# Optimization experiments

Measured on AMD Instinct MI355X. Metric: run time of the kernel, lower is better.

The kernel has to match this reference:

```python
import jax, jax.numpy as jnp
import numpy as np

N1, N2, C, G1, G2 = 20000, 80000, 64, 128, 256
K = 27


def _nbr_map(coords, key, G):
    # coords sorted by key = x*G*G + y*G + z; returns [M,27] neighbor idx, -1 if absent
    M = coords.shape[0]
    nbr = np.full((M, K), -1, np.int32)
    k = 0
    for dx in (-1, 0, 1):
        for dy in (-1, 0, 1):
            for dz in (-1, 0, 1):
                nc = coords + np.array([dx, dy, dz])
                valid = np.all((nc >= 0) & (nc < G), axis=1)
                nk = nc[:, 0] * G * G + nc[:, 1] * G + nc[:, 2]
                pos = np.clip(np.searchsorted(key, nk), 0, M - 1)
                hit = valid & (key[pos] == nk)
                nbr[:, k] = np.where(hit, pos, -1)
                k += 1
    return nbr


def setup_inputs() -> dict:
    rng = np.random.default_rng(0)
    # --- parent (curr) level: unique sorted voxels on 128^3 grid ---
    lin = np.sort(rng.choice(G1 ** 3, size=N1, replace=False))
    cc = np.stack([lin // (G1 * G1), (lin // G1) % G1, lin % G1], axis=1)
    # occupancy codes with exactly 4 set bits -> exactly 4 children per parent
    bits4 = np.argsort(rng.random((N1, 8)), axis=1)[:, :4]  # [N1,4]
    curr_occ = (1 << bits4).sum(axis=1).astype(np.int32)[:, None]
    # --- FCG expansion: child coords = parent*2 + octant offset ---
    off = np.stack([(bits4 >> 2) & 1, (bits4 >> 1) & 1, bits4 & 1], axis=-1)
    child = (cc[:, None, :] * 2 + off).reshape(-1, 3)
    parent_idx = np.repeat(np.arange(N1, dtype=np.int32), 4)
    ckey = child[:, 0] * G2 * G2 + child[:, 1] * G2 + child[:, 2]
    o = np.argsort(ckey)  # op.sort_CF
    child, parent_idx, ckey = child[o], parent_idx[o], ckey[o]
    next_octant = ((child[:, 0] % 2) * 4 + (child[:, 1] % 2) * 2 + (child[:, 2] % 2)).astype(np.int32)
    next_occ = rng.integers(0, 256, size=(N2, 1)).astype(np.int32)
    nbr_curr = _nbr_map(cc, lin, G1)
    nbr_next = _nbr_map(child, ckey, G2)

    key = jax.random.key(0)
    ks = jax.random.split(key, 16)
    f32 = jnp.float32
    inp = {
        'prior_emb': jax.random.normal(ks[0], (256, C), f32),
        'target_emb8': jax.random.normal(ks[1], (8, C), f32),
        'Wp': jax.random.normal(ks[2], (5, K, C, C), f32) * 0.03,
        'Wt': jax.random.normal(ks[3], (5, K, C, C), f32) * 0.03,
        'W0a': jax.random.normal(ks[4], (C, C), f32) * 0.1,
        'b0a': jnp.zeros((C,), f32),
        'W0b': jax.random.normal(ks[5], (C, 16), f32) * 0.1,
        'b0b': jnp.zeros((16,), f32),
        'W1a': jax.random.normal(ks[6], (C, C), f32) * 0.1,
        'b1a': jnp.zeros((C,), f32),
        'W1b': jax.random.normal(ks[7], (C, 16), f32) * 0.1,
        'b1b': jnp.zeros((16,), f32),
        's1_emb': jax.random.normal(ks[8], (16, C), f32),
        'curr_occ': jnp.asarray(curr_occ),
        'next_occ': jnp.asarray(next_occ),
        'next_octant': jnp.asarray(next_octant),
        'parent_idx': jnp.asarray(parent_idx),
        'nbr_curr': jnp.asarray(nbr_curr),
        'nbr_next': jnp.asarray(nbr_next),
        'n_points': 640000,
    }
    return inp


def _sp_conv(feats, nbr, W):
    # 3x3x3 sparse conv via kernel map: out[i] = sum_k feats[nbr[i,k]] @ W[k]
    out = jnp.zeros((feats.shape[0], W.shape[-1]), feats.dtype)
    for k in range(K):
        idx = nbr[:, k]
        g = jnp.where((idx >= 0)[:, None], feats[jnp.clip(idx, 0, None)], 0.0)
        out = out + g @ W[k]
    return out


def _resnet(feats, nbr, Wa, Wb):
    h = jax.nn.relu(_sp_conv(feats, nbr, Wa))
    h = _sp_conv(h, nbr, Wb)
    return jax.nn.relu(feats + h)


def reference(prior_emb, target_emb8, Wp, Wt, W0a, b0a, W0b, b0b, W1a, b1a, W1b, b1b, s1_emb,
              curr_occ, next_occ, next_octant, parent_idx, nbr_curr, nbr_next, n_points):
    # prior branch on parent level
    f = prior_emb[curr_occ[:, 0]]                              # [N1,C]
    f = jax.nn.relu(_sp_conv(f, nbr_curr, Wp[0]))
    f = _resnet(f, nbr_curr, Wp[1], Wp[2])
    f = _resnet(f, nbr_curr, Wp[3], Wp[4])
    # FCG: broadcast parent feats to children, add octant (target) embedding
    g = f[parent_idx] + target_emb8[next_octant]               # [N2,C]
    g = jax.nn.relu(_sp_conv(g, nbr_next, Wt[0]))
    g = _resnet(g, nbr_next, Wt[1], Wt[2])
    g = _resnet(g, nbr_next, Wt[3], Wt[4])
    # bit-prediction heads
    lower = jnp.remainder(next_occ, 16)                        # [N2,1]
    upper = next_occ // 16                                     # [N2,1]
    lp = jax.nn.softmax(jax.nn.relu(g @ W0a + b0a) @ W0b + b0b, axis=-1)
    h1 = g + s1_emb[lower[:, 0]]
    up = jax.nn.softmax(jax.nn.relu(h1 @ W1a + b1a) @ W1b + b1b, axis=-1)
    lp_gt = jnp.take_along_axis(lp, lower, axis=1)
    up_gt = jnp.take_along_axis(up, upper, axis=1)
    eps = 1e-10
    bits = jnp.sum(jnp.clip(-jnp.log2(lp_gt + eps), 0.0, 50.0))
    bits = bits + jnp.sum(jnp.clip(-jnp.log2(up_gt + eps), 0.0, 50.0))
    return bits / n_points
```

## Files before the change

### kernel.cpp

```cpp
#include <hip/hip_runtime.h>

#define NP1 20000
#define NP2 80000
#define KN  27

typedef unsigned short ushort;
typedef unsigned int   uint;
typedef __attribute__((ext_vector_type(8))) short short8v;
typedef __attribute__((ext_vector_type(4))) float f32x4;

__device__ __forceinline__ ushort f2bf(float x) {
    union { float f; uint u; } v; v.f = x;
    uint r = v.u + 0x7fffu + ((v.u >> 16) & 1u);
    return (ushort)(r >> 16);
}
__device__ __forceinline__ float bf2f(ushort s) {
    union { uint u; float f; } v; v.u = ((uint)s) << 16;
    return v.f;
}
__device__ __forceinline__ void gload_lds16(const void* g, void* l) {
    __builtin_amdgcn_global_load_lds(
        (const __attribute__((address_space(1))) unsigned int*)g,
        (__attribute__((address_space(3))) unsigned int*)l, 16, 0, 0);
}
__device__ __forceinline__ int xcd_swz(int b, int nb) {
    int q = nb >> 3, r = nb & 7;
    int x = b & 7, p = b >> 3;
    return (x < r) ? x * (q + 1) + p : r * (q + 1) + (x - r) * q + p;
}

__global__ __launch_bounds__(256) void prep_wT_tile_k(
    const float* __restrict__ Wp, const float* __restrict__ Wt,
    ushort* __restrict__ dstp, ushort* __restrict__ dstt)
{
    __shared__ float sT[64 * 65];
    int b = blockIdx.x;
    const float* W = (b < 135) ? Wp : Wt;
    ushort* dst    = (b < 135) ? dstp : dstt;
    int k = (b < 135) ? b : b - 135;
    const float* src = W + (size_t)k * 4096;
    int t = threadIdx.x;
    #pragma unroll
    for (int p = 0; p < 16; ++p) {
        int i = t + p * 256;
        sT[(i >> 6) * 65 + (i & 63)] = src[i];
    }
    __syncthreads();
    ushort* d = dst + (size_t)k * 4096;
    #pragma unroll
    for (int p = 0; p < 16; ++p) {
        int o = t + p * 256;
        int c = o >> 6, jj = o & 63;
        int j = (((jj >> 3) ^ (c & 7)) << 3) | (jj & 7);
        d[o] = f2bf(sT[j * 65 + c]);
    }
}

__global__ __launch_bounds__(256) void prep_small_k(
    const float* __restrict__ W0a, const float* __restrict__ W1a,
    const float* __restrict__ W0b, const float* __restrict__ W1b,
    const float* __restrict__ s1,
    ushort* __restrict__ W0aT, ushort* __restrict__ W1aT,
    ushort* __restrict__ W0bT, ushort* __restrict__ W1bT,
    ushort* __restrict__ s1bT)
{
    int b = blockIdx.x, t = threadIdx.x;
    if (b < 32) {
        const float* W = (b < 16) ? W0a : W1a;
        ushort* dst    = (b < 16) ? W0aT : W1aT;
        int i = (b & 15) * 256 + t;
        int c = i >> 6, jj = i & 63;
        int j = (((jj >> 3) ^ (c & 7)) << 3) | (jj & 7);
        dst[i] = f2bf(W[j * 64 + c]);
    } else if (b < 40) {
        const float* W = (b < 36) ? W0b : W1b;
        ushort* dst    = (b < 36) ? W0bT : W1bT;
        int i = (b - ((b < 36) ? 32 : 36)) * 256 + t;
        int c = i >> 6, jj = i & 63;
        int j = (((jj >> 3) ^ (c & 7)) << 3) | (jj & 7);
        dst[i] = f2bf(W[j * 16 + c]);
    } else {
        int i = (b - 40) * 256 + t;
        int e = i >> 6, jj = i & 63;
        int j = (((jj >> 3) ^ (e & 7)) << 3) | (jj & 7);
        s1bT[i] = f2bf(s1[e * 64 + j]);
    }
}

__global__ __launch_bounds__(256) void gather_curr_k(
    const float* __restrict__ prior_emb, const int* __restrict__ curr_occ,
    ushort* __restrict__ out)
{
    int i = blockIdx.x * 256 + threadIdx.x;
    if (i >= NP1 * 32) return;
    int row = i >> 5, cp = (i & 31) * 2;
    const float* src = prior_emb + (size_t)curr_occ[row] * 64 + cp;
    uint pk = (uint)f2bf(src[0]) | ((uint)f2bf(src[1]) << 16);
    *(uint*)((char*)out + (size_t)row * 128 + cp * 2) = pk;
}

__global__ __launch_bounds__(256) void gather_next_k(
    const ushort* __restrict__ f, const int* __restrict__ parent_idx,
    const int* __restrict__ next_oct, const float* __restrict__ temb8,
    ushort* __restrict__ out)
{
    int i = blockIdx.x * 256 + threadIdx.x;
    if (i >= NP2 * 32) return;
    int row = i >> 5, cp = (i & 31) * 2;
    const ushort* fs = f + (size_t)parent_idx[row] * 64 + cp;
    const float* ts = temb8 + (size_t)next_oct[row] * 64 + cp;
    float v0 = bf2f(fs[0]) + ts[0];
    float v1 = bf2f(fs[1]) + ts[1];
    uint pk = (uint)f2bf(v0) | ((uint)f2bf(v1) << 16);
    *(uint*)((char*)out + (size_t)row * 128 + cp * 2) = pk;
}

template<int NW, int CG>
__global__ __launch_bounds__(NW * 64) void spconv_reg_k(
    const ushort* __restrict__ feats, const int* __restrict__ nbr,
    const ushort* __restrict__ Wsw, const ushort* __restrict__ res,
    ushort* __restrict__ out, const ushort* __restrict__ zpage, int nblocks)
{
    constexpr int ROWS   = (NW / CG) * 16;
    constexpr int NB     = 4 / CG;
    constexpr int WLOADS = 8192 / (NW * 64 * 16);

    __shared__ __align__(16) char sW[2 * 8192];

    const int t = threadIdx.x;
    const int w = t >> 6, l = t & 63;
    const int wg = xcd_swz(blockIdx.x, nblocks);
    const int row0 = wg * ROWS;
    const int lr = l & 15, lhi = l >> 4;
    const int colbase = (w % CG) * (NB * 16);
    const int rw = w / CG;
    const int ch0 = lhi ^ (lr & 7);
    const int ch1 = (4 + lhi) ^ (lr & 7);

    const int* nbrow = nbr + (size_t)(row0 + rw * 16 + lr) * KN;

    f32x4 acc[NB];
    #pragma unroll
    for (int b = 0; b < NB; ++b) acc[b] = (f32x4)0.0f;

    short8v aC0, aC1, aN0, aN1;
    int idxA, idxB;

    #define LOADA(IDX, CHOFF) \
        (*(const short8v*)(((IDX) >= 0 ? (const char*)feats + (size_t)(IDX) * 128 \
                                       : (const char*)zpage) + ((CHOFF) + lhi) * 16))

    {
        int id0 = nbrow[0];
        aC0 = LOADA(id0, 0);
        aC1 = LOADA(id0, 4);
        idxA = nbrow[1];
        const char* wsrc = (const char*)Wsw;
        #pragma unroll
        for (int i = 0; i < WLOADS; ++i) {
            int off = (w * WLOADS + i) * 1024;
            gload_lds16(wsrc + off + l * 16, sW + off);
        }
    }

    for (int k = 0; k < KN; ++k) {
        char* cur = sW + (k & 1) * 8192;
        char* nxt = sW + ((k + 1) & 1) * 8192;

        __syncthreads();

        if (k < KN - 1) {
            const char* wsrc = (const char*)Wsw + (size_t)(k + 1) * 8192;
            #pragma unroll
            for (int i = 0; i < WLOADS; ++i) {
                int off = (w * WLOADS + i) * 1024;
                gload_lds16(wsrc + off + l * 16, nxt + off);
            }
            aN0 = LOADA(idxA, 0);
            aN1 = LOADA(idxA, 4);
        }
        if (k < KN - 2) idxB = nbrow[k + 2];

        __builtin_amdgcn_s_setprio(1);
        {
            short8v b0[NB];
            #pragma unroll
            for (int nb = 0; nb < NB; ++nb)
                b0[nb] = *(const short8v*)(cur + (colbase + nb * 16 + lr) * 128 + ch0 * 16);
            #pragma unroll
            for (int nb = 0; nb < NB; ++nb)
                acc[nb] = __builtin_amdgcn_mfma_f32_16x16x32_bf16(aC0, b0[nb], acc[nb], 0, 0, 0);
            short8v b1[NB];
            #pragma unroll
            for (int nb = 0; nb < NB; ++nb)
                b1[nb] = *(const short8v*)(cur + (colbase + nb * 16 + lr) * 128 + ch1 * 16);
            #pragma unroll
            for (int nb = 0; nb < NB; ++nb)
                acc[nb] = __builtin_amdgcn_mfma_f32_16x16x32_bf16(aC1, b1[nb], acc[nb], 0, 0, 0);
        }
        __builtin_amdgcn_s_setprio(0);

        aC0 = aN0; aC1 = aN1; idxA = idxB;
    }
    #undef LOADA

    #pragma unroll
    for (int nb = 0; nb < NB; ++nb) {
        #pragma unroll
        for (int r = 0; r < 4; ++r) {
            int rg = row0 + rw * 16 + lhi * 4 + r;
            int c = colbase + nb * 16 + lr;
            float v = acc[nb][r];
            if (res != nullptr) v += bf2f(res[(size_t)rg * 64 + c]);
            v = fmaxf(v, 0.0f);
            float o = __shfl_xor(v, 1);
            if (!(l & 1)) {
                uint pk = (uint)f2bf(v) | ((uint)f2bf(o) << 16);
                *(uint*)((char*)out + (size_t)rg * 128 + (c << 1)) = pk;
            }
        }
    }
}

__global__ __launch_bounds__(512) void head_v2_k(
    const ushort* __restrict__ G, const int* __restrict__ next_occ,
    const ushort* __restrict__ Wsmall,
    const float* __restrict__ b0a, const float* __restrict__ b1a,
    const float* __restrict__ b0b, const float* __restrict__ b1b,
    const int* __restrict__ n_points, float* __restrict__ outp)
{
    __shared__ __align__(16) char sm[48288];
    char*  sWs = sm;
    char*  sHb = sm + 22528;
    float* sLb = (float*)(sm + 38912);
    float* sBf = (float*)(sm + 47616);
    float* sRed = (float*)(sm + 48256);

    const int t = threadIdx.x;
    const int w = t >> 6, l = t & 63;
    const int row0 = blockIdx.x * 128;
    const int lr = l & 15, lhi = l >> 4;
    char*  sH = sHb + w * 2048;
    float* sL = sLb + w * 272;

    const int myrow = row0 + w * 16 + lr;
    const int occ_l = next_occ[myrow];

    short8v aG0 = *(const short8v*)((const char*)G + (size_t)myrow * 128 + lhi * 16);
    short8v aG1 = *(const short8v*)((const char*)G + (size_t)myrow * 128 + (4 + lhi) * 16);

    for (int i = w; i < 22; i += 8)
        gload_lds16((const char*)Wsmall + i * 1024 + l * 16, sWs + i * 1024);
    if (t < 64)       sBf[t] = b0a[t];
    else if (t < 128) sBf[t] = b1a[t - 64];
    else if (t < 144) sBf[128 + (t - 128)] = b0b[t - 128];
    else if (t < 160) sBf[144 + (t - 144)] = b1b[t - 144];
    __syncthreads();

    float bacc = 0.0f;

    {
        f32x4 a0[4];
        #pragma unroll
        for (int b = 0; b < 4; ++b) a0[b] = (f32x4)0.0f;
        #pragma unroll
        for (int j0 = 0; j0 < 2; ++j0) {
            short8v a = j0 ? aG1 : aG0;
            #pragma unroll
            for (int nb = 0; nb < 4; ++nb) {
                int c = nb * 16 + lr;
                int ch = (j0 * 4 + lhi) ^ (c & 7);
                short8v b = *(const short8v*)(sWs + c * 128 + ch * 16);
                a0[nb] = __builtin_amdgcn_mfma_f32_16x16x32_bf16(a, b, a0[nb], 0, 0, 0);
            }
        }
        #pragma unroll
        for (int nb = 0; nb < 4; ++nb) {
            float bias = sBf[nb * 16 + lr];
            #pragma unroll
            for (int r = 0; r < 4; ++r) {
                int row = lhi * 4 + r;
                int j = nb * 16 + lr;
                float v = fmaxf(a0[nb][r] + bias, 0.0f);
                float o = __shfl_xor(v, 1);
                if (!(l & 1)) {
                    uint pk = (uint)f2bf(v) | ((uint)f2bf(o) << 16);
                    *(uint*)(sH + row * 128 + (((j >> 3) ^ (row & 7)) << 4)
                             + (j & 7) * 2) = pk;
                }
            }
        }
        asm volatile("s_waitcnt lgkmcnt(0)" ::: "memory");
        __builtin_amdgcn_sched_barrier(0);
        f32x4 lg = (f32x4)0.0f;
        #pragma unroll
        for (int j0 = 0; j0 < 2; ++j0) {
            int ch = (j0 * 4 + lhi) ^ (lr & 7);
            short8v a = *(const short8v*)(sH + lr * 128 + ch * 16);
            short8v b = *(const short8v*)(sWs + 16384 + lr * 128 + ch * 16);
            lg = __builtin_amdgcn_mfma_f32_16x16x32_bf16(a, b, lg, 0, 0, 0);
        }
        #pragma unroll
        for (int r = 0; r < 4; ++r)
            sL[(lhi * 4 + r) * 17 + lr] = lg[r] + sBf[128 + lr];
        asm volatile("s_waitcnt lgkmcnt(0)" ::: "memory");
        __builtin_amdgcn_sched_barrier(0);
        {
            int tgt = occ_l & 15;
            float lv[16], mx = -1e30f;
            #pragma unroll
            for (int c = 0; c < 16; ++c) {
                lv[c] = sL[lr * 17 + c];
                mx = fmaxf(mx, lv[c]);
            }
            float ssum = 0.0f, lt = lv[0];
            #pragma unroll
            for (int c = 0; c < 16; ++c) {
                ssum += __expf(lv[c] - mx);
                lt = (c == tgt) ? lv[c] : lt;
            }
            float p = __expf(lt - mx) / ssum;
            float bits = fminf(fmaxf(-log2f(p + 1e-10f), 0.0f), 50.0f);
            if (l < 16) bacc += bits;
        }
    }

    {
        f32x4 a1[4];
        #pragma unroll
        for (int b = 0; b < 4; ++b) a1[b] = (f32x4)0.0f;
        int low_l = occ_l & 15;
        #pragma unroll
        for (int j0 = 0; j0 < 2; ++j0) {
            short8v g8 = j0 ? aG1 : aG0;
            int che = (j0 * 4 + lhi) ^ (low_l & 7);
            short8v e8 = *(const short8v*)(sWs + 20480 + low_l * 128 + che * 16);
            short8v a;
            #pragma unroll
            for (int e = 0; e < 8; ++e) {
                float f = bf2f((ushort)g8[e]) + bf2f((ushort)e8[e]);
                a[e] = (short)f2bf(f);
            }
            #pragma unroll
            for (int nb = 0; nb < 4; ++nb) {
                int c = nb * 16 + lr;
                int ch = (j0 * 4 + lhi) ^ (c & 7);
                short8v b = *(const short8v*)(sWs + 8192 + c * 128 + ch * 16);
                a1[nb] = __builtin_amdgcn_mfma_f32_16x16x32_bf16(a, b, a1[nb], 0, 0, 0);
            }
        }
        #pragma unroll
        for (int nb = 0; nb < 4; ++nb) {
            float bias = sBf[64 + nb * 16 + lr];
            #pragma unroll
            for (int r = 0; r < 4; ++r) {
                int row = lhi * 4 + r;
                int j = nb * 16 + lr;
                float v = fmaxf(a1[nb][r] + bias, 0.0f);
                float o = __shfl_xor(v, 1);
                if (!(l & 1)) {
                    uint pk = (uint)f2bf(v) | ((uint)f2bf(o) << 16);
                    *(uint*)(sH + row * 128 + (((j >> 3) ^ (row & 7)) << 4)
                             + (j & 7) * 2) = pk;
                }
            }
        }
        asm volatile("s_waitcnt lgkmcnt(0)" ::: "memory");
        __builtin_amdgcn_sched_barrier(0);
        f32x4 lg = (f32x4)0.0f;
        #pragma unroll
        for (int j0 = 0; j0 < 2; ++j0) {
            int ch = (j0 * 4 + lhi) ^ (lr & 7);
            short8v a = *(const short8v*)(sH + lr * 128 + ch * 16);
            short8v b = *(const short8v*)(sWs + 18432 + lr * 128 + ch * 16);
            lg = __builtin_amdgcn_mfma_f32_16x16x32_bf16(a, b, lg, 0, 0, 0);
        }
        #pragma unroll
        for (int r = 0; r < 4; ++r)
            sL[(lhi * 4 + r) * 17 + lr] = lg[r] + sBf[144 + lr];
        asm volatile("s_waitcnt lgkmcnt(0)" ::: "memory");
        __builtin_amdgcn_sched_barrier(0);
        {
            int tgt = occ_l >> 4;
            float lv[16], mx = -1e30f;
            #pragma unroll
            for (int c = 0; c < 16; ++c) {
                lv[c] = sL[lr * 17 + c];
                mx = fmaxf(mx, lv[c]);
            }
            float ssum = 0.0f, lt = lv[0];
            #pragma unroll
            for (int c = 0; c < 16; ++c) {
                ssum += __expf(lv[c] - mx);
                lt = (c == tgt) ? lv[c] : lt;
            }
            float p = __expf(lt - mx) / ssum;
            float bits = fminf(fmaxf(-log2f(p + 1e-10f), 0.0f), 50.0f);
            if (l < 16) bacc += bits;
        }
    }

    #pragma unroll
    for (int s = 1; s < 64; s <<= 1) bacc += __shfl_xor(bacc, s);
    if (l == 0) sRed[w] = bacc;
    __syncthreads();
    if (t == 0) {
        float s = 0.0f;
        #pragma unroll
        for (int i = 0; i < 8; ++i) s += sRed[i];
        atomicAdd(outp, s / (float)(*n_points));
    }
}

extern "C" void kernel_launch(void* const* d_in, const int* in_sizes, int n_in,
                              void* d_out, int out_size, void* d_ws, size_t ws_size,
                              hipStream_t stream)
{
    const float* prior_emb = (const float*)d_in[0];
    const float* temb8     = (const float*)d_in[1];
    const float* Wp        = (const float*)d_in[2];
    const float* Wt        = (const float*)d_in[3];
    const float* W0a       = (const float*)d_in[4];
    const float* b0a       = (const float*)d_in[5];
    const float* W0b       = (const float*)d_in[6];
    const float* b0b       = (const float*)d_in[7];
    const float* W1a       = (const float*)d_in[8];
    const float* b1a       = (const float*)d_in[9];
    const float* W1b       = (const float*)d_in[10];
    const float* b1b       = (const float*)d_in[11];
    const float* s1_emb    = (const float*)d_in[12];
    const int*   curr_occ  = (const int*)d_in[13];
    const int*   next_occ  = (const int*)d_in[14];
    const int*   next_oct  = (const int*)d_in[15];
    const int*   parent    = (const int*)d_in[16];
    const int*   nbr_curr  = (const int*)d_in[17];
    const int*   nbr_next  = (const int*)d_in[18];
    const int*   n_points  = (const int*)d_in[19];
    float* out = (float*)d_out;

    char* wsb = (char*)d_ws;
    ushort* zpage = (ushort*)wsb;
    size_t off = 256;
    ushort* WpT = (ushort*)(wsb + off); off += (size_t)135 * 4096 * 2;
    ushort* WtT = (ushort*)(wsb + off); off += (size_t)135 * 4096 * 2;
    ushort* Wsmall = (ushort*)(wsb + off);
    ushort* W0aT = Wsmall;
    ushort* W1aT = Wsmall + 4096;
    ushort* W0bT = Wsmall + 8192;
    ushort* W1bT = Wsmall + 9216;
    ushort* s1bT = Wsmall + 10240;
    off += 11264 * 2;
    off = (off + 255) & ~(size_t)255;
    ushort* fA = (ushort*)(wsb + off); off += (size_t)NP1 * 64 * 2;
    ushort* fB = (ushort*)(wsb + off); off += (size_t)NP1 * 64 * 2;
    ushort* fC = (ushort*)(wsb + off); off += (size_t)NP1 * 64 * 2;
    ushort* gA = (ushort*)(wsb + off); off += (size_t)NP2 * 64 * 2;
    ushort* gB = (ushort*)(wsb + off); off += (size_t)NP2 * 64 * 2;
    ushort* gC = (ushort*)(wsb + off); off += (size_t)NP2 * 64 * 2;

    hipMemsetAsync(d_out, 0, sizeof(float), stream);
    hipMemsetAsync(zpage, 0, 256, stream);

    prep_wT_tile_k<<<270, 256, 0, stream>>>(Wp, Wt, WpT, WtT);
    prep_small_k<<<44, 256, 0, stream>>>(W0a, W1a, W0b, W1b, s1_emb,
                                         W0aT, W1aT, W0bT, W1bT, s1bT);

    gather_curr_k<<<(NP1 * 32 + 255) / 256, 256, 0, stream>>>(prior_emb, curr_occ, fA);

    const size_t WT = (size_t)KN * 4096;
    spconv_reg_k<4,2><<<625, 256, 0, stream>>>(fA, nbr_curr, WpT + 0 * WT, nullptr, fB, zpage, 625);
    spconv_reg_k<4,2><<<625, 256, 0, stream>>>(fB, nbr_curr, WpT + 1 * WT, nullptr, fC, zpage, 625);
    spconv_reg_k<4,2><<<625, 256, 0, stream>>>(fC, nbr_curr, WpT + 2 * WT, fB,      fA, zpage, 625);
    spconv_reg_k<4,2><<<625, 256, 0, stream>>>(fA, nbr_curr, WpT + 3 * WT, nullptr, fC, zpage, 625);
    spconv_reg_k<4,2><<<625, 256, 0, stream>>>(fC, nbr_curr, WpT + 4 * WT, fA,      fB, zpage, 625);

    gather_next_k<<<(NP2 * 32 + 255) / 256, 256, 0, stream>>>(fB, parent, next_oct, temb8, gA);

    spconv_reg_k<8,1><<<625, 512, 0, stream>>>(gA, nbr_next, WtT + 0 * WT, nullptr, gB, zpage, 625);
    spconv_reg_k<8,1><<<625, 512, 0, stream>>>(gB, nbr_next, WtT + 1 * WT, nullptr, gC, zpage, 625);
    spconv_reg_k<8,1><<<625, 512, 0, stream>>>(gC, nbr_next, WtT + 2 * WT, gB,      gA, zpage, 625);
    spconv_reg_k<8,1><<<625, 512, 0, stream>>>(gA, nbr_next, WtT + 3 * WT, nullptr, gC, zpage, 625);
    spconv_reg_k<8,1><<<625, 512, 0, stream>>>(gC, nbr_next, WtT + 4 * WT, gA,      gB, zpage, 625);

    head_v2_k<<<625, 512, 0, stream>>>(gB, next_occ, Wsmall,
                                       b0a, b1a, b0b, b1b, n_points, out);
}
```

Baseline: 258.8 us.

## Load sparse-conv weights directly from global into registers, dropping LDS staging

The sparse convolution kernel stops staging per-offset weight tiles in LDS with double buffering and block-wide barriers. Each wave now loads its B fragments straight from global memory (which should stay L2-resident) into registers, using a two-stage even/odd software pipeline across the 27 kernel offsets. The next-level convs switch to 256-thread blocks with twice as many blocks, and the kernel gets an occupancy hint of 4 blocks per CU. This removes the barriers and LDS traffic but raises global/L2 load traffic and register pressure, since every wave fetches the weights itself.

Measured after the change: 646.0 us. 150% more time.

```diff
diff --git a/kernel.cpp b/kernel.cpp
--- a/kernel.cpp
+++ b/kernel.cpp
@@ -115,17 +115,14 @@
     *(uint*)((char*)out + (size_t)row * 128 + cp * 2) = pk;
 }
 
-template<int NW, int CG>
-__global__ __launch_bounds__(NW * 64) void spconv_reg_k(
+template<int CG>
+__global__ __launch_bounds__(256, 4) void spconv_nolds_k(
     const ushort* __restrict__ feats, const int* __restrict__ nbr,
     const ushort* __restrict__ Wsw, const ushort* __restrict__ res,
     ushort* __restrict__ out, const ushort* __restrict__ zpage, int nblocks)
 {
-    constexpr int ROWS   = (NW / CG) * 16;
-    constexpr int NB     = 4 / CG;
-    constexpr int WLOADS = 8192 / (NW * 64 * 16);
-
-    __shared__ __align__(16) char sW[2 * 8192];
+    constexpr int NB   = 4 / CG;
+    constexpr int ROWS = (4 / CG) * 16;
 
     const int t = threadIdx.x;
     const int w = t >> 6, l = t & 63;
@@ -134,75 +131,77 @@
     const int lr = l & 15, lhi = l >> 4;
     const int colbase = (w % CG) * (NB * 16);
     const int rw = w / CG;
-    const int ch0 = lhi ^ (lr & 7);
-    const int ch1 = (4 + lhi) ^ (lr & 7);
-
-    const int* nbrow = nbr + (size_t)(row0 + rw * 16 + lr) * KN;
+    const int myrow = row0 + rw * 16 + lr;
+    const int* nbrow = nbr + (size_t)myrow * KN;
+    const char* wbase = (const char*)Wsw;
+
+    int boff[2][NB];
+    #pragma unroll
+    for (int j0 = 0; j0 < 2; ++j0)
+        #pragma unroll
+        for (int nb = 0; nb < NB; ++nb) {
+            int c = colbase + nb * 16 + lr;
+            boff[j0][nb] = c * 128 + (((j0 * 4 + lhi) ^ (c & 7)) << 4);
+        }
 
     f32x4 acc[NB];
     #pragma unroll
     for (int b = 0; b < NB; ++b) acc[b] = (f32x4)0.0f;
 
-    short8v aC0, aC1, aN0, aN1;
-    int idxA, idxB;
+    short8v Ae0, Ae1, Ao0, Ao1;
+    short8v Be[2][NB], Bo[2][NB];
+    int idxO, idxE;
 
     #define LOADA(IDX, CHOFF) \
         (*(const short8v*)(((IDX) >= 0 ? (const char*)feats + (size_t)(IDX) * 128 \
                                        : (const char*)zpage) + ((CHOFF) + lhi) * 16))
+    #define LOADB(DST, K)                                                        \
+        _Pragma("unroll")                                                        \
+        for (int j0 = 0; j0 < 2; ++j0)                                           \
+            _Pragma("unroll")                                                    \
+            for (int nb = 0; nb < NB; ++nb)                                      \
+                DST[j0][nb] = *(const short8v*)(wbase + (size_t)(K) * 8192       \
+                                                + boff[j0][nb]);
+    #define COMPUTE(A0, A1, B)                                                   \
+        __builtin_amdgcn_s_setprio(1);                                           \
+        _Pragma("unroll")                                                        \
+        for (int nb = 0; nb < NB; ++nb)                                          \
+            acc[nb] = __builtin_amdgcn_mfma_f32_16x16x32_bf16(A0, B[0][nb],      \
+                                                              acc[nb], 0, 0, 0); \
+        _Pragma("unroll")                                                        \
+        for (int nb = 0; nb < NB; ++nb)                                          \
+            acc[nb] = __builtin_amdgcn_mfma_f32_16x16x32_bf16(A1, B[1][nb],      \
+                                                              acc[nb], 0, 0, 0); \
+        __builtin_amdgcn_s_setprio(0);
 
     {
         int id0 = nbrow[0];
-        aC0 = LOADA(id0, 0);
-        aC1 = LOADA(id0, 4);
-        idxA = nbrow[1];
-        const char* wsrc = (const char*)Wsw;
-        #pragma unroll
-        for (int i = 0; i < WLOADS; ++i) {
-            int off = (w * WLOADS + i) * 1024;
-            gload_lds16(wsrc + off + l * 16, sW + off);
-        }
-    }
-
-    for (int k = 0; k < KN; ++k) {
-        char* cur = sW + (k & 1) * 8192;
-        char* nxt = sW + ((k + 1) & 1) * 8192;
-
-        __syncthreads();
-
-        if (k < KN - 1) {
-            const char* wsrc = (const char*)Wsw + (size_t)(k + 1) * 8192;
-            #pragma unroll
-            for (int i = 0; i < WLOADS; ++i) {
-                int off = (w * WLOADS + i) * 1024;
-                gload_lds16(wsrc + off + l * 16, nxt + off);
-            }
-            aN0 = LOADA(idxA, 0);
-            aN1 = LOADA(idxA, 4);
-        }
-        if (k < KN - 2) idxB = nbrow[k + 2];
-
-        __builtin_amdgcn_s_setprio(1);
-        {
-            short8v b0[NB];
-            #pragma unroll
-            for (int nb = 0; nb < NB; ++nb)
-                b0[nb] = *(const short8v*)(cur + (colbase + nb * 16 + lr) * 128 + ch0 * 16);
-            #pragma unroll
-            for (int nb = 0; nb < NB; ++nb)
-                acc[nb] = __builtin_amdgcn_mfma_f32_16x16x32_bf16(aC0, b0[nb], acc[nb], 0, 0, 0);
-            short8v b1[NB];
-            #pragma unroll
-            for (int nb = 0; nb < NB; ++nb)
-                b1[nb] = *(const short8v*)(cur + (colbase + nb * 16 + lr) * 128 + ch1 * 16);
-            #pragma unroll
-            for (int nb = 0; nb < NB; ++nb)
-                acc[nb] = __builtin_amdgcn_mfma_f32_16x16x32_bf16(aC1, b1[nb], acc[nb], 0, 0, 0);
-        }
-        __builtin_amdgcn_s_setprio(0);
-
-        aC0 = aN0; aC1 = aN1; idxA = idxB;
-    }
+        Ae0 = LOADA(id0, 0);
+        Ae1 = LOADA(id0, 4);
+        LOADB(Be, 0);
+        idxO = nbrow[1];
+        idxE = nbrow[2];
+    }
+
+    #pragma unroll 1
+    for (int kp = 0; kp < 13; ++kp) {
+        const int k = 2 * kp;
+        Ao0 = LOADA(idxO, 0);
+        Ao1 = LOADA(idxO, 4);
+        LOADB(Bo, k + 1);
+        if (kp < 12) idxO = nbrow[k + 3];
+        COMPUTE(Ae0, Ae1, Be);
+        Ae0 = LOADA(idxE, 0);
+        Ae1 = LOADA(idxE, 4);
+        LOADB(Be, k + 2);
+        if (kp < 12) idxE = nbrow[k + 4];
+        COMPUTE(Ao0, Ao1, Bo);
+    }
+    COMPUTE(Ae0, Ae1, Be);
+
     #undef LOADA
+    #undef LOADB
+    #undef COMPUTE
 
     #pragma unroll
     for (int nb = 0; nb < NB; ++nb) {
@@ -468,19 +467,19 @@
     gather_curr_k<<<(NP1 * 32 + 255) / 256, 256, 0, stream>>>(prior_emb, curr_occ, fA);
 
     const size_t WT = (size_t)KN * 4096;
-    spconv_reg_k<4,2><<<625, 256, 0, stream>>>(fA, nbr_curr, WpT + 0 * WT, nullptr, fB, zpage, 625);
-    spconv_reg_k<4,2><<<625, 256, 0, stream>>>(fB, nbr_curr, WpT + 1 * WT, nullptr, fC, zpage, 625);
-    spconv_reg_k<4,2><<<625, 256, 0, stream>>>(fC, nbr_curr, WpT + 2 * WT, fB,      fA, zpage, 625);
-    spconv_reg_k<4,2><<<625, 256, 0, stream>>>(fA, nbr_curr, WpT + 3 * WT, nullptr, fC, zpage, 625);
-    spconv_reg_k<4,2><<<625, 256, 0, stream>>>(fC, nbr_curr, WpT + 4 * WT, fA,      fB, zpage, 625);
+    spconv_nolds_k<2><<<625, 256, 0, stream>>>(fA, nbr_curr, WpT + 0 * WT, nullptr, fB, zpage, 625);
+    spconv_nolds_k<2><<<625, 256, 0, stream>>>(fB, nbr_curr, WpT + 1 * WT, nullptr, fC, zpage, 625);
+    spconv_nolds_k<2><<<625, 256, 0, stream>>>(fC, nbr_curr, WpT + 2 * WT, fB,      fA, zpage, 625);
+    spconv_nolds_k<2><<<625, 256, 0, stream>>>(fA, nbr_curr, WpT + 3 * WT, nullptr, fC, zpage, 625);
+    spconv_nolds_k<2><<<625, 256, 0, stream>>>(fC, nbr_curr, WpT + 4 * WT, fA,      fB, zpage, 625);
 
     gather_next_k<<<(NP2 * 32 + 255) / 256, 256, 0, stream>>>(fB, parent, next_oct, temb8, gA);
 
-    spconv_reg_k<8,1><<<625, 512, 0, stream>>>(gA, nbr_next, WtT + 0 * WT, nullptr, gB, zpage, 625);
-    spconv_reg_k<8,1><<<625, 512, 0, stream>>>(gB, nbr_next, WtT + 1 * WT, nullptr, gC, zpage, 625);
-    spconv_reg_k<8,1><<<625, 512, 0, stream>>>(gC, nbr_next, WtT + 2 * WT, gB,      gA, zpage, 625);
-    spconv_reg_k<8,1><<<625, 512, 0, stream>>>(gA, nbr_next, WtT + 3 * WT, nullptr, gC, zpage, 625);
-    spconv_reg_k<8,1><<<625, 512, 0, stream>>>(gC, nbr_next, WtT + 4 * WT, gA,      gB, zpage, 625);
+    spconv_nolds_k<1><<<1250, 256, 0, stream>>>(gA, nbr_next, WtT + 0 * WT, nullptr, gB, zpage, 1250);
+    spconv_nolds_k<1><<<1250, 256, 0, stream>>>(gB, nbr_next, WtT + 1 * WT, nullptr, gC, zpage, 1250);
+    spconv_nolds_k<1><<<1250, 256, 0, stream>>>(gC, nbr_next, WtT + 2 * WT, gB,      gA, zpage, 1250);
+    spconv_nolds_k<1><<<1250, 256, 0, stream>>>(gA, nbr_next, WtT + 3 * WT, nullptr, gC, zpage, 1250);
+    spconv_nolds_k<1><<<1250, 256, 0, stream>>>(gC, nbr_next, WtT + 4 * WT, gA,      gB, zpage, 1250);
 
     head_v2_k<<<625, 512, 0, stream>>>(gB, next_occ, Wsmall,
                                        b0a, b1a, b0b, b1b, n_points, out);
```

## Add triple-buffered weight pipeline kernel for next-level sparse convs

Applied to the files above, without the earlier changes.

Adds a new sparse-conv kernel for the 80k-row level. It triple-buffers the per-tap weight tiles in LDS and prefetches neighbour feature rows two taps ahead, using explicit vmcnt waits and one barrier per tap. The aim is to hide global load latency for both weights and gathered features behind the MFMA work, replacing the previous double-buffered scheme. It costs more LDS and registers per block, which may lower occupancy. The existing kernel also gains an MB template parameter, which is set to 1 everywhere.

Result: slower. 296.7 us (+14.6%).

```diff
diff --git a/kernel.cpp b/kernel.cpp
--- a/kernel.cpp
+++ b/kernel.cpp
@@ -22,6 +22,12 @@
     __builtin_amdgcn_global_load_lds(
         (const __attribute__((address_space(1))) unsigned int*)g,
         (__attribute__((address_space(3))) unsigned int*)l, 16, 0, 0);
+}
+template<int N> __device__ __forceinline__ void wait_vmcnt() {
+    if constexpr (N == 0)      asm volatile("s_waitcnt vmcnt(0)" ::: "memory");
+    else if constexpr (N == 2) asm volatile("s_waitcnt vmcnt(2)" ::: "memory");
+    else if constexpr (N == 4) asm volatile("s_waitcnt vmcnt(4)" ::: "memory");
+    else if constexpr (N == 5) asm volatile("s_waitcnt vmcnt(5)" ::: "memory");
 }
 __device__ __forceinline__ int xcd_swz(int b, int nb) {
     int q = nb >> 3, r = nb & 7;
@@ -115,13 +121,13 @@
     *(uint*)((char*)out + (size_t)row * 128 + cp * 2) = pk;
 }
 
-template<int NW, int CG>
+template<int NW, int MB, int CG>
 __global__ __launch_bounds__(NW * 64) void spconv_reg_k(
     const ushort* __restrict__ feats, const int* __restrict__ nbr,
     const ushort* __restrict__ Wsw, const ushort* __restrict__ res,
     ushort* __restrict__ out, const ushort* __restrict__ zpage, int nblocks)
 {
-    constexpr int ROWS   = (NW / CG) * 16;
+    constexpr int ROWS   = (NW / CG) * MB * 16;
     constexpr int NB     = 4 / CG;
     constexpr int WLOADS = 8192 / (NW * 64 * 16);
 
@@ -137,7 +143,7 @@
     const int ch0 = lhi ^ (lr & 7);
     const int ch1 = (4 + lhi) ^ (lr & 7);
 
-    const int* nbrow = nbr + (size_t)(row0 + rw * 16 + lr) * KN;
+    const int* nbrow = nbr + (size_t)(row0 + rw * MB * 16 + lr) * KN;
 
     f32x4 acc[NB];
     #pragma unroll
@@ -208,8 +214,115 @@
     for (int nb = 0; nb < NB; ++nb) {
         #pragma unroll
         for (int r = 0; r < 4; ++r) {
-            int rg = row0 + rw * 16 + lhi * 4 + r;
+            int rg = row0 + rw * MB * 16 + lhi * 4 + r;
             int c = colbase + nb * 16 + lr;
+            float v = acc[nb][r];
+            if (res != nullptr) v += bf2f(res[(size_t)rg * 64 + c]);
+            v = fmaxf(v, 0.0f);
+            float o = __shfl_xor(v, 1);
+            if (!(l & 1)) {
+                uint pk = (uint)f2bf(v) | ((uint)f2bf(o) << 16);
+                *(uint*)((char*)out + (size_t)rg * 128 + (c << 1)) = pk;
+            }
+        }
+    }
+}
+
+__global__ __launch_bounds__(512) void spconv_pipe3_k(
+    const ushort* __restrict__ feats, const int* __restrict__ nbr,
+    const ushort* __restrict__ Wsw, const ushort* __restrict__ res,
+    ushort* __restrict__ out, const ushort* __restrict__ zpage, int nblocks)
+{
+    constexpr int ROWS = 128;
+
+    __shared__ __align__(16) char sW[3 * 8192];
+
+    const int t = threadIdx.x;
+    const int w = t >> 6, l = t & 63;
+    const int wg = xcd_swz(blockIdx.x, nblocks);
+    const int row0 = wg * ROWS;
+    const int lr = l & 15, lhi = l >> 4;
+    const int ch0 = lhi ^ (lr & 7);
+    const int ch1 = (4 + lhi) ^ (lr & 7);
+
+    const int* nbrow = nbr + (size_t)(row0 + w * 16 + lr) * KN;
+
+    f32x4 acc[4];
+    #pragma unroll
+    for (int b = 0; b < 4; ++b) acc[b] = (f32x4)0.0f;
+
+    short8v A0[2], A1[2], A2[2];
+    int i0, i1, i2;
+
+    #define LOADA(IDX, CHOFF) \
+        (*(const short8v*)(((IDX) >= 0 ? (const char*)feats + (size_t)(IDX) * 128 \
+                                       : (const char*)zpage) + ((CHOFF) + lhi) * 16))
+
+    {
+        int id0 = nbrow[0];
+        A0[0] = LOADA(id0, 0); A0[1] = LOADA(id0, 4);
+        int id1 = nbrow[1];
+        A1[0] = LOADA(id1, 0); A1[1] = LOADA(id1, 4);
+        gload_lds16((const char*)Wsw + w * 1024 + l * 16, sW + w * 1024);
+        gload_lds16((const char*)Wsw + 8192 + w * 1024 + l * 16, sW + 8192 + w * 1024);
+        i2 = nbrow[2];
+        asm volatile("" ::: "memory");
+    }
+
+#define P3_TAP(K, P, WBUF, WN, DOA, DOW, DOI, ACUR, AIN, IIN, IOUT)            \
+    {                                                                          \
+        const int k_ = (K);                                                    \
+        wait_vmcnt<WN>();                                                      \
+        __builtin_amdgcn_s_barrier();                                          \
+        __builtin_amdgcn_sched_barrier(0);                                     \
+        if (DOA) { AIN[0] = LOADA(IIN, 0); AIN[1] = LOADA(IIN, 4); }           \
+        if (DOW) {                                                             \
+            const char* ws = (const char*)Wsw + (size_t)(k_ + 2) * 8192;       \
+            gload_lds16(ws + w * 1024 + l * 16, sW + (WBUF) * 8192 + w * 1024);\
+        }                                                                      \
+        if (DOI) { IOUT = nbrow[k_ + 3]; }                                     \
+        __builtin_amdgcn_s_setprio(1);                                         \
+        {                                                                      \
+            const char* cur = sW + (P) * 8192;                                 \
+            short8v b0[4];                                                     \
+            _Pragma("unroll")                                                  \
+            for (int nb = 0; nb < 4; ++nb)                                     \
+                b0[nb] = *(const short8v*)(cur + (nb * 16 + lr) * 128 + ch0 * 16); \
+            _Pragma("unroll")                                                  \
+            for (int nb = 0; nb < 4; ++nb)                                     \
+                acc[nb] = __builtin_amdgcn_mfma_f32_16x16x32_bf16(             \
+                    ACUR[0], b0[nb], acc[nb], 0, 0, 0);                        \
+            short8v b1[4];                                                     \
+            _Pragma("unroll")                                                  \
+            for (int nb = 0; nb < 4; ++nb)                                     \
+                b1[nb] = *(const short8v*)(cur + (nb * 16 + lr) * 128 + ch1 * 16); \
+            _Pragma("unroll")                                                  \
+            for (int nb = 0; nb < 4; ++nb)                                     \
+                acc[nb] = __builtin_amdgcn_mfma_f32_16x16x32_bf16(             \
+                    ACUR[1], b1[nb], acc[nb], 0, 0, 0);                        \
+        }                                                                      \
+        __builtin_amdgcn_s_setprio(0);                                         \
+    }
+
+    P3_TAP(0, 0, 2, 2, true, true, true, A0, A2, i2, i0)
+    #pragma unroll 1
+    for (int kp = 0; kp < 8; ++kp) {
+        int kb = 3 * kp;
+        P3_TAP(kb + 1, 1, 0, 5, true, true, (kb + 1) < 24, A1, A0, i0, i1)
+        P3_TAP(kb + 2, 2, 1, 5, true, true, (kb + 2) < 24, A2, A1, i1, i2)
+        P3_TAP(kb + 3, 0, 2, 5, true, true, (kb + 3) < 24, A0, A2, i2, i0)
+    }
+    P3_TAP(25, 1, 0, 4, false, false, false, A1, A0, i0, i1)
+    P3_TAP(26, 2, 1, 0, false, false, false, A2, A1, i1, i2)
+#undef P3_TAP
+    #undef LOADA
+
+    #pragma unroll
+    for (int nb = 0; nb < 4; ++nb) {
+        #pragma unroll
+        for (int r = 0; r < 4; ++r) {
+            int rg = row0 + w * 16 + lhi * 4 + r;
+            int c = nb * 16 + lr;
             float v = acc[nb][r];
             if (res != nullptr) v += bf2f(res[(size_t)rg * 64 + c]);
             v = fmaxf(v, 0.0f);
@@ -468,19 +581,19 @@
     gather_curr_k<<<(NP1 * 32 + 255) / 256, 256, 0, stream>>>(prior_emb, curr_occ, fA);
 
     const size_t WT = (size_t)KN * 4096;
-    spconv_reg_k<4,2><<<625, 256, 0, stream>>>(fA, nbr_curr, WpT + 0 * WT, nullptr, fB, zpage, 625);
-    spconv_reg_k<4,2><<<625, 256, 0, stream>>>(fB, nbr_curr, WpT + 1 * WT, nullptr, fC, zpage, 625);
-    spconv_reg_k<4,2><<<625, 256, 0, stream>>>(fC, nbr_curr, WpT + 2 * WT, fB,      fA, zpage, 625);
-    spconv_reg_k<4,2><<<625, 256, 0, stream>>>(fA, nbr_curr, WpT + 3 * WT, nullptr, fC, zpage, 625);
-    spconv_reg_k<4,2><<<625, 256, 0, stream>>>(fC, nbr_curr, WpT + 4 * WT, fA,      fB, zpage, 625);
+    spconv_reg_k<4,1,2><<<625, 256, 0, stream>>>(fA, nbr_curr, WpT + 0 * WT, nullptr, fB, zpage, 625);
+    spconv_reg_k<4,1,2><<<625, 256, 0, stream>>>(fB, nbr_curr, WpT + 1 * WT, nullptr, fC, zpage, 625);
+    spconv_reg_k<4,1,2><<<625, 256, 0, stream>>>(fC, nbr_curr, WpT + 2 * WT, fB,      fA, zpage, 625);
+    spconv_reg_k<4,1,2><<<625, 256, 0, stream>>>(fA, nbr_curr, WpT + 3 * WT, nullptr, fC, zpage, 625);
+    spconv_reg_k<4,1,2><<<625, 256, 0, stream>>>(fC, nbr_curr, WpT + 4 * WT, fA,      fB, zpage, 625);
 
     gather_next_k<<<(NP2 * 32 + 255) / 256, 256, 0, stream>>>(fB, parent, next_oct, temb8, gA);
 
-    spconv_reg_k<8,1><<<625, 512, 0, stream>>>(gA, nbr_next, WtT + 0 * WT, nullptr, gB, zpage, 625);
-    spconv_reg_k<8,1><<<625, 512, 0, stream>>>(gB, nbr_next, WtT + 1 * WT, nullptr, gC, zpage, 625);
-    spconv_reg_k<8,1><<<625, 512, 0, stream>>>(gC, nbr_next, WtT + 2 * WT, gB,      gA, zpage, 625);
-    spconv_reg_k<8,1><<<625, 512, 0, stream>>>(gA, nbr_next, WtT + 3 * WT, nullptr, gC, zpage, 625);
-    spconv_reg_k<8,1><<<625, 512, 0, stream>>>(gC, nbr_next, WtT + 4 * WT, gA,      gB, zpage, 625);
+    spconv_pipe3_k<<<625, 512, 0, stream>>>(gA, nbr_next, WtT + 0 * WT, nullptr, gB, zpage, 625);
+    spconv_pipe3_k<<<625, 512, 0, stream>>>(gB, nbr_next, WtT + 1 * WT, nullptr, gC, zpage, 625);
+    spconv_pipe3_k<<<625, 512, 0, stream>>>(gC, nbr_next, WtT + 2 * WT, gB,      gA, zpage, 625);
+    spconv_pipe3_k<<<625, 512, 0, stream>>>(gA, nbr_next, WtT + 3 * WT, nullptr, gC, zpage, 625);
+    spconv_pipe3_k<<<625, 512, 0, stream>>>(gC, nbr_next, WtT + 4 * WT, gA,      gB, zpage, 625);
 
     head_v2_k<<<625, 512, 0, stream>>>(gB, next_occ, Wsmall,
                                        b0a, b1a, b0b, b1b, n_points, out);
```
